# Performance work log

Measured on AMD Instinct MI355X. Metric: run time of the kernel, lower is better.

Reference implementation:

```python
import jax, jax.numpy as jnp
import numpy as np
from jax import lax

BETA = 0.9
THRESHOLD = 1.0
SLOPE = 25.0
TIME_STEPS = 50


@jax.custom_vjp
def spike(u):
    # Heaviside forward; fast_sigmoid surrogate backward
    return (u > 0).astype(u.dtype)

def _spike_fwd(u):
    return spike(u), u

def _spike_bwd(u, g):
    return (g / (SLOPE * jnp.abs(u) + 1.0) ** 2,)

spike.defvjp(_spike_fwd, _spike_bwd)


def setup_inputs() -> dict:
    key = jax.random.key(0)
    k = jax.random.split(key, 5)
    B, D_IN, D_H, D_OUT = 1024, 1024, 2048, 256
    return {
        "x": jax.random.normal(k[0], (B, D_IN), jnp.float32),
        "W1": jax.random.normal(k[1], (D_H, D_IN), jnp.float32) / np.sqrt(D_IN),
        "b1": jax.random.normal(k[2], (D_H,), jnp.float32) * 0.01,
        "W2": jax.random.normal(k[3], (D_OUT, D_H), jnp.float32) / np.sqrt(D_H),
        "b2": jax.random.normal(k[4], (D_OUT,), jnp.float32) * 0.01,
    }


def reference(x, W1, b1, W2, b2):
    # fc1(x) is constant across time steps (static input) -> hoist out of scan
    cur1 = x @ W1.T + b1  # [B, H]
    B = x.shape[0]
    H, O = W1.shape[0], W2.shape[0]
    dt = x.dtype

    def step(carry, _):
        mem1, mem2, h_sum, out_sum = carry
        # snntorch Leaky, subtract reset: reset based on PREVIOUS mem, detached
        reset1 = lax.stop_gradient((mem1 > THRESHOLD).astype(dt))
        mem1 = BETA * mem1 + cur1 - reset1 * THRESHOLD
        spk1 = spike(mem1 - THRESHOLD)
        cur2 = spk1 @ W2.T + b2  # [B, O]
        reset2 = lax.stop_gradient((mem2 > THRESHOLD).astype(dt))
        mem2 = BETA * mem2 + cur2 - reset2 * THRESHOLD
        spk2 = spike(mem2 - THRESHOLD)
        return (mem1, mem2, h_sum + spk1, out_sum + spk2), None

    init = (jnp.zeros((B, H), dt), jnp.zeros((B, O), dt),
            jnp.zeros((B, H), dt), jnp.zeros((B, O), dt))
    (mem1, mem2, h_sum, out_sum), _ = lax.scan(step, init, None, length=TIME_STEPS)
    return (h_sum, out_sum)
```

## Files before the change

kernel.cpp:

```cpp
#include <hip/hip_runtime.h>
#include <stdint.h>


#define BATCH 1024
#define DIN   1024
#define DH    2048
#define DOUT  256
#define TSTEPS 50
#define QS    131072.0f
#define QINVS 7.62939453125e-6f

typedef __bf16 bf16x8 __attribute__((ext_vector_type(8)));
typedef float  f32x4  __attribute__((ext_vector_type(4)));
typedef int    i32x4  __attribute__((ext_vector_type(4)));
typedef int    i32x16 __attribute__((ext_vector_type(16)));

__device__ __forceinline__ void gl2lds16(const void* g, void* l) {
  __builtin_amdgcn_global_load_lds(
      (const __attribute__((address_space(1))) uint32_t*)(uintptr_t)g,
      (__attribute__((address_space(3))) uint32_t*)(uint32_t)(uintptr_t)l,
      16, 0, 0);
}

__device__ __forceinline__ uint16_t f32_bf16_rne(float f) {
  uint32_t u = __float_as_uint(f);
  uint32_t r = u + 0x7FFFu + ((u >> 16) & 1u);
  return (uint16_t)(r >> 16);
}

__global__ void prep_kernel(const float* __restrict__ x, const float* __restrict__ W1,
                            const float* __restrict__ W2,
                            uint16_t* __restrict__ PXh, uint16_t* __restrict__ PXl,
                            uint16_t* __restrict__ PWh, uint16_t* __restrict__ PWl,
                            int8_t* __restrict__ PB) {
  int bid = blockIdx.x;
  if (bid < 1536) {
    const float* src;
    uint16_t *dh, *dl;
    int m, ko; size_t M;
    if (bid < 512) {
      int t = bid * 256 + threadIdx.x;
      m = t >> 7; ko = t & 127; M = 1024;
      src = x + (size_t)m * DIN + ko * 8;
      dh = PXh; dl = PXl;
    } else {
      int t = (bid - 512) * 256 + threadIdx.x;
      m = t >> 7; ko = t & 127; M = 2048;
      src = W1 + (size_t)m * DIN + ko * 8;
      dh = PWh; dl = PWl;
    }
    float4 a = *(const float4*)(src);
    float4 b = *(const float4*)(src + 4);
    float v[8] = {a.x, a.y, a.z, a.w, b.x, b.y, b.z, b.w};
    uint16_t h[8], l[8];
#pragma unroll
    for (int j = 0; j < 8; ++j) {
      h[j] = f32_bf16_rne(v[j]);
      l[j] = f32_bf16_rne(v[j] - __uint_as_float((uint32_t)h[j] << 16));
    }
    size_t o = ((size_t)ko * M + m) * 8;
    *(uint4*)(dh + o) = make_uint4(h[0] | (h[1] << 16), h[2] | (h[3] << 16),
                                   h[4] | (h[5] << 16), h[6] | (h[7] << 16));
    *(uint4*)(dl + o) = make_uint4(l[0] | (l[1] << 16), l[2] | (l[3] << 16),
                                   l[4] | (l[5] << 16), l[6] | (l[7] << 16));
  } else {
    int t = (bid - 1536) * 256 + threadIdx.x;
    int k0 = (t & 127) * 16;
    int n = t >> 7;
    uint32_t hw[4], lw[4];
#pragma unroll
    for (int g = 0; g < 4; ++g) {
      float4 v = *(const float4*)(W2 + (size_t)n * DH + k0 + g * 4);
      float vv[4] = {v.x, v.y, v.z, v.w};
      uint32_t hb = 0, lb = 0;
#pragma unroll
      for (int j = 0; j < 4; ++j) {
        int q = (int)rintf(vv[j] * QS);
        int h = (q + 128) >> 8;
        int l = q - (h << 8);
        hb |= ((uint32_t)(uint8_t)(int8_t)h) << (8 * j);
        lb |= ((uint32_t)(uint8_t)(int8_t)l) << (8 * j);
      }
      hw[g] = hb; lw[g] = lb;
    }
    int kc = k0 >> 5, kh = (k0 >> 4) & 1, nb = n >> 5;
    int lane = (n & 31) + 32 * kh;
    size_t off = (((size_t)(kc * 8 + nb) * 2 + 0) * 64 + lane) * 16;
    *(uint4*)(PB + off)        = make_uint4(hw[0], hw[1], hw[2], hw[3]);
    *(uint4*)(PB + off + 1024) = make_uint4(lw[0], lw[1], lw[2], lw[3]);
  }
}

__global__ __launch_bounds__(256, 4) void gemm1_kernel(
    const uint16_t* __restrict__ PXh, const uint16_t* __restrict__ PXl,
    const uint16_t* __restrict__ PWh, const uint16_t* __restrict__ PWl,
    const float* __restrict__ bias, float* __restrict__ C) {
  const int K = DIN, N = DH;
  __shared__ uint16_t sAh[2048], sAl[2048], sBh[2048], sBl[2048];
  int tid = threadIdx.x;
  int lane = tid & 63, wave = tid >> 6;
  int wm = (wave >> 1) * 32, wn = (wave & 1) * 32;
  int m0 = blockIdx.x * 64, n0 = blockIdx.y * 64;
  int rf = lane & 15;
  int ko = lane >> 4;

  f32x4 acc[2][2] = {};

  int sko = tid >> 6, srow = tid & 63;

  for (int k0 = 0; k0 < K; k0 += 32) {
    size_t oa = ((size_t)((k0 >> 3) + sko) * 1024 + m0 + srow) * 8;
    size_t ob = ((size_t)((k0 >> 3) + sko) * 2048 + n0 + srow) * 8;
    gl2lds16(PXh + oa, &sAh[tid * 8]);
    gl2lds16(PXl + oa, &sAl[tid * 8]);
    gl2lds16(PWh + ob, &sBh[tid * 8]);
    gl2lds16(PWl + ob, &sBl[tid * 8]);
    __syncthreads();

    bf16x8 ah[2], al[2], bh[2], bl[2];
#pragma unroll
    for (int i = 0; i < 2; ++i) {
      int ra = (ko * 64 + wm + i * 16 + rf) * 8;
      ah[i] = *(const bf16x8*)&sAh[ra];
      al[i] = *(const bf16x8*)&sAl[ra];
      int rb = (ko * 64 + wn + i * 16 + rf) * 8;
      bh[i] = *(const bf16x8*)&sBh[rb];
      bl[i] = *(const bf16x8*)&sBl[rb];
    }
#pragma unroll
    for (int i = 0; i < 2; ++i)
#pragma unroll
      for (int j = 0; j < 2; ++j) {
        acc[i][j] = __builtin_amdgcn_mfma_f32_16x16x32_bf16(ah[i], bh[j], acc[i][j], 0, 0, 0);
        acc[i][j] = __builtin_amdgcn_mfma_f32_16x16x32_bf16(ah[i], bl[j], acc[i][j], 0, 0, 0);
        acc[i][j] = __builtin_amdgcn_mfma_f32_16x16x32_bf16(al[i], bh[j], acc[i][j], 0, 0, 0);
      }
    __syncthreads();
  }

  int cq = (lane >> 4) * 4;
#pragma unroll
  for (int j = 0; j < 2; ++j) {
    int col = n0 + wn + j * 16 + rf;
    float bv = bias[col];
#pragma unroll
    for (int i = 0; i < 2; ++i) {
      size_t row = m0 + wm + i * 16 + cq;
      float* cp = C + row * N + col;
#pragma unroll
      for (int r = 0; r < 4; ++r) cp[(size_t)r * N] = acc[i][j][r] + bv;
    }
  }
}

__global__ __launch_bounds__(512, 2) void gemm2_kernel(
    const int8_t* __restrict__ PA, const int8_t* __restrict__ PB,
    const float* __restrict__ bias, float* __restrict__ C, int RB) {
  int tid = threadIdx.x;
  int lane = tid & 63, wave = tid >> 6;
  int wmh = wave >> 2;
  int wnq = wave & 3;
  int bx = blockIdx.x;
  int mb0 = bx * 4 + wmh * 2;

  const int8_t* pa = PA + ((size_t)mb0 * 64 + lane) * 16;
  const int8_t* pb = PB + ((size_t)wnq * 4 * 64 + lane) * 16;
  size_t strideA = (size_t)RB * 1024;

  i32x16 acch[2][2] = {};
  i32x16 accl[2][2] = {};

  i32x4 ab[4][2], bb[4][4];
#pragma unroll
  for (int u = 0; u < 4; ++u) {
    ab[u][0] = *(const i32x4*)(pa);
    ab[u][1] = *(const i32x4*)(pa + 1024);
    bb[u][0] = *(const i32x4*)(pb);
    bb[u][1] = *(const i32x4*)(pb + 1024);
    bb[u][2] = *(const i32x4*)(pb + 2048);
    bb[u][3] = *(const i32x4*)(pb + 3072);
    pa += strideA; pb += 16384;
  }
  __builtin_amdgcn_sched_barrier(0);

  for (int kc0 = 0; kc0 < 64; kc0 += 4) {
#pragma unroll
    for (int u = 0; u < 4; ++u) {
      acch[0][0] = __builtin_amdgcn_mfma_i32_32x32x32_i8(ab[u][0], bb[u][0], acch[0][0], 0, 0, 0);
      accl[0][0] = __builtin_amdgcn_mfma_i32_32x32x32_i8(ab[u][0], bb[u][1], accl[0][0], 0, 0, 0);
      acch[0][1] = __builtin_amdgcn_mfma_i32_32x32x32_i8(ab[u][0], bb[u][2], acch[0][1], 0, 0, 0);
      accl[0][1] = __builtin_amdgcn_mfma_i32_32x32x32_i8(ab[u][0], bb[u][3], accl[0][1], 0, 0, 0);
      acch[1][0] = __builtin_amdgcn_mfma_i32_32x32x32_i8(ab[u][1], bb[u][0], acch[1][0], 0, 0, 0);
      accl[1][0] = __builtin_amdgcn_mfma_i32_32x32x32_i8(ab[u][1], bb[u][1], accl[1][0], 0, 0, 0);
      acch[1][1] = __builtin_amdgcn_mfma_i32_32x32x32_i8(ab[u][1], bb[u][2], acch[1][1], 0, 0, 0);
      accl[1][1] = __builtin_amdgcn_mfma_i32_32x32x32_i8(ab[u][1], bb[u][3], accl[1][1], 0, 0, 0);
      __builtin_amdgcn_sched_barrier(0);
      ab[u][0] = *(const i32x4*)(pa);
      ab[u][1] = *(const i32x4*)(pa + 1024);
      bb[u][0] = *(const i32x4*)(pb);
      bb[u][1] = *(const i32x4*)(pb + 1024);
      bb[u][2] = *(const i32x4*)(pb + 2048);
      bb[u][3] = *(const i32x4*)(pb + 3072);
      pa += strideA; pb += 16384;
      __builtin_amdgcn_sched_barrier(0);
    }
  }

  int rm = lane & 31, half = lane >> 5;
#pragma unroll
  for (int mi = 0; mi < 2; ++mi)
#pragma unroll
    for (int ni = 0; ni < 2; ++ni) {
      int col = wnq * 64 + ni * 32 + rm;
      float bv = bias[col];
#pragma unroll
      for (int r = 0; r < 16; ++r) {
        int row = bx * 128 + wmh * 64 + mi * 32 + (r & 3) + 8 * (r >> 2) + 4 * half;
        int q = acch[mi][ni][r] * 256 + accl[mi][ni][r];
        C[(size_t)row * DOUT + col] = (float)q * QINVS + bv;
      }
    }
}

__global__ void lif1_kernel(const float* __restrict__ cur1, float* __restrict__ mem1,
                            int8_t* __restrict__ PA, float* __restrict__ hsum,
                            int tc, int init, int save_mem, int RB) {
#pragma clang fp contract(off)
  int idx = blockIdx.x * 256 + threadIdx.x;
  int b = idx & 1023;
  int h0 = (idx >> 10) * 16;
  size_t e0 = (size_t)b * DH + h0;

  float m[16], c[16], hs[16];
#pragma unroll
  for (int g = 0; g < 4; ++g) {
    float4 v = *(const float4*)(cur1 + e0 + g * 4);
    c[g * 4] = v.x; c[g * 4 + 1] = v.y; c[g * 4 + 2] = v.z; c[g * 4 + 3] = v.w;
  }
#pragma unroll
  for (int v = 0; v < 16; ++v) { m[v] = 0.0f; hs[v] = 0.0f; }
  if (!init) {
#pragma unroll
    for (int g = 0; g < 4; ++g) {
      float4 v = *(const float4*)(mem1 + e0 + g * 4);
      m[g * 4] = v.x; m[g * 4 + 1] = v.y; m[g * 4 + 2] = v.z; m[g * 4 + 3] = v.w;
    }
  }

  int kc = h0 >> 5, kh = (h0 >> 4) & 1;
  int lane = (b & 31) + 32 * kh;
  int8_t* pa = PA + (((size_t)kc * RB + (b >> 5)) * 64 + lane) * 16;

  for (int t = 0; t < tc; ++t) {
    uint32_t w[4] = {0, 0, 0, 0};
#pragma unroll
    for (int v = 0; v < 16; ++v) {
      float r = (m[v] > 1.0f) ? 1.0f : 0.0f;
      m[v] = 0.9f * m[v] + c[v] - r;
      bool s = (m[v] - 1.0f) > 0.0f;
      hs[v] += s ? 1.0f : 0.0f;
      w[v >> 2] |= (s ? 1u : 0u) << (8 * (v & 3));
    }
    *(uint4*)(pa + (size_t)t * 32768) = make_uint4(w[0], w[1], w[2], w[3]);
  }

  if (save_mem) {
#pragma unroll
    for (int g = 0; g < 4; ++g)
      *(float4*)(mem1 + e0 + g * 4) = make_float4(m[g * 4], m[g * 4 + 1], m[g * 4 + 2], m[g * 4 + 3]);
  }
  if (init) {
#pragma unroll
    for (int g = 0; g < 4; ++g)
      *(float4*)(hsum + e0 + g * 4) = make_float4(hs[g * 4], hs[g * 4 + 1], hs[g * 4 + 2], hs[g * 4 + 3]);
  } else {
#pragma unroll
    for (int g = 0; g < 4; ++g) {
      float4 v = *(float4*)(hsum + e0 + g * 4);
      v.x += hs[g * 4]; v.y += hs[g * 4 + 1]; v.z += hs[g * 4 + 2]; v.w += hs[g * 4 + 3];
      *(float4*)(hsum + e0 + g * 4) = v;
    }
  }
}

__global__ void lif2_kernel(const float* __restrict__ cur2, float* __restrict__ mem2,
                            float* __restrict__ osum, int tc, int init, int save_mem) {
#pragma clang fp contract(off)
  int idx = blockIdx.x * 256 + threadIdx.x;
  int e = idx * 4;
  float m[4], os[4];
  if (init) { m[0] = m[1] = m[2] = m[3] = 0.0f; }
  else { float4 v = *(const float4*)(mem2 + e); m[0] = v.x; m[1] = v.y; m[2] = v.z; m[3] = v.w; }
  os[0] = os[1] = os[2] = os[3] = 0.0f;
  for (int t = 0; t < tc; ++t) {
    float4 cv = *(const float4*)(cur2 + (size_t)t * (BATCH * DOUT) + e);
    float c[4] = {cv.x, cv.y, cv.z, cv.w};
#pragma unroll
    for (int v = 0; v < 4; ++v) {
      float r = (m[v] > 1.0f) ? 1.0f : 0.0f;
      m[v] = 0.9f * m[v] + c[v] - r;
      os[v] += ((m[v] - 1.0f) > 0.0f) ? 1.0f : 0.0f;
    }
  }
  if (save_mem) *(float4*)(mem2 + e) = make_float4(m[0], m[1], m[2], m[3]);
  if (init) {
    *(float4*)(osum + e) = make_float4(os[0], os[1], os[2], os[3]);
  } else {
    float4 v = *(float4*)(osum + e);
    v.x += os[0]; v.y += os[1]; v.z += os[2]; v.w += os[3];
    *(float4*)(osum + e) = v;
  }
}

extern "C" void kernel_launch(void* const* d_in, const int* in_sizes, int n_in,
                              void* d_out, int out_size, void* d_ws, size_t ws_size,
                              hipStream_t stream) {
  const float* x  = (const float*)d_in[0];
  const float* W1 = (const float*)d_in[1];
  const float* b1 = (const float*)d_in[2];
  const float* W2 = (const float*)d_in[3];
  const float* b2 = (const float*)d_in[4];
  float* out = (float*)d_out;
  char* ws = (char*)d_ws;

  const size_t fixed = 40 * 1024 * 1024;
  int tc = 10;
  if (ws_size >= fixed + 50ull * (2097152 + 1048576)) tc = 50;
  else if (ws_size >= fixed + 25ull * (2097152 + 1048576)) tc = 25;
  int nchunk = TSTEPS / tc;
  int RB = tc * 32;

  size_t off = 0;
  auto alloc = [&](size_t b) { size_t p = off; off = (off + b + 255) & ~(size_t)255; return p; };
  uint16_t* PXh  = (uint16_t*)(ws + alloc(2097152));
  uint16_t* PXl  = (uint16_t*)(ws + alloc(2097152));
  uint16_t* PWh  = (uint16_t*)(ws + alloc(4194304));
  uint16_t* PWl  = (uint16_t*)(ws + alloc(4194304));
  int8_t*   PB   = (int8_t*)(ws + alloc(1048576 + 65536));
  float*    cur1 = (float*)(ws + alloc(8388608));
  float*    mem1 = (float*)(ws + alloc(8388608));
  float*    mem2 = (float*)(ws + alloc(1048576));
  int8_t*   PA   = (int8_t*)(ws + alloc((size_t)tc * BATCH * DH + 4ull * RB * 1024));
  float*    cur2c = (float*)(ws + alloc((size_t)tc * BATCH * DOUT * 4));

  if (nchunk > 1) {
    hipMemsetAsync(mem1, 0, 8388608, stream);
    hipMemsetAsync(mem2, 0, 1048576, stream);
  }

  prep_kernel<<<1664, 256, 0, stream>>>(x, W1, W2, PXh, PXl, PWh, PWl, PB);

  gemm1_kernel<<<dim3(BATCH / 64, DH / 64), 256, 0, stream>>>(PXh, PXl, PWh, PWl, b1, cur1);

  int save = (nchunk > 1) ? 1 : 0;
  for (int c = 0; c < nchunk; ++c) {
    int init = (c == 0) ? 1 : 0;
    lif1_kernel<<<(BATCH * DH) / (256 * 16), 256, 0, stream>>>(
        cur1, mem1, PA, out, tc, init, save, RB);
    gemm2_kernel<<<(tc * BATCH) / 128, 512, 0, stream>>>(
        PA, PB, b2, cur2c, RB);
    lif2_kernel<<<(BATCH * DOUT) / (256 * 4), 256, 0, stream>>>(
        cur2c, mem2, out + BATCH * DH, tc, init, save);
  }
}
```

Before: 202.7 us.

## Bit-pack spike matrix and drop LDS staging in first GEMM

The spike activations passed from the LIF1 stage to the second GEMM are now stored as 16-bit bitmasks instead of one byte per spike. The GEMM expands them back into int8 MFMA operands in registers with a multiply-and-mask trick. This cuts the spike buffer traffic by a factor of eight in exchange for some extra ALU work per MFMA. Separately, gemm1 now loads its operands straight from global memory into registers with a two-stage software prefetch, with no LDS staging and no block barriers, and its launch bounds change. The workspace sizing is adjusted to match.

```diff
diff --git a/kernel.cpp b/kernel.cpp
--- a/kernel.cpp
+++ b/kernel.cpp
@@ -15,17 +15,19 @@
 typedef int    i32x4  __attribute__((ext_vector_type(4)));
 typedef int    i32x16 __attribute__((ext_vector_type(16)));
 
-__device__ __forceinline__ void gl2lds16(const void* g, void* l) {
-  __builtin_amdgcn_global_load_lds(
-      (const __attribute__((address_space(1))) uint32_t*)(uintptr_t)g,
-      (__attribute__((address_space(3))) uint32_t*)(uint32_t)(uintptr_t)l,
-      16, 0, 0);
-}
-
 __device__ __forceinline__ uint16_t f32_bf16_rne(float f) {
   uint32_t u = __float_as_uint(f);
   uint32_t r = u + 0x7FFFu + ((u >> 16) & 1u);
   return (uint16_t)(r >> 16);
+}
+
+__device__ __forceinline__ i32x4 expand16(uint32_t s) {
+  i32x4 r;
+  r[0] = (int)((( s        & 0xFu) * 0x00204081u) & 0x01010101u);
+  r[1] = (int)((((s >>  4) & 0xFu) * 0x00204081u) & 0x01010101u);
+  r[2] = (int)((((s >>  8) & 0xFu) * 0x00204081u) & 0x01010101u);
+  r[3] = (int)((((s >> 12) & 0xFu) * 0x00204081u) & 0x01010101u);
+  return r;
 }
 
 __global__ void prep_kernel(const float* __restrict__ x, const float* __restrict__ W1,
@@ -91,61 +93,73 @@
   }
 }
 
-__global__ __launch_bounds__(256, 4) void gemm1_kernel(
+__global__ __launch_bounds__(256, 2) void gemm1_kernel(
     const uint16_t* __restrict__ PXh, const uint16_t* __restrict__ PXl,
     const uint16_t* __restrict__ PWh, const uint16_t* __restrict__ PWl,
     const float* __restrict__ bias, float* __restrict__ C) {
-  const int K = DIN, N = DH;
-  __shared__ uint16_t sAh[2048], sAl[2048], sBh[2048], sBl[2048];
+  const int N = DH;
   int tid = threadIdx.x;
   int lane = tid & 63, wave = tid >> 6;
   int wm = (wave >> 1) * 32, wn = (wave & 1) * 32;
-  int m0 = blockIdx.x * 64, n0 = blockIdx.y * 64;
+  int m0 = blockIdx.x * 64 + wm;
+  int n0 = blockIdx.y * 64 + wn;
   int rf = lane & 15;
   int ko = lane >> 4;
+  const int AK = 4 * 1024 * 8;
+  const int BK = 4 * 2048 * 8;
+
+  const uint16_t* axh = PXh + ((size_t)ko * 1024 + m0 + rf) * 8;
+  const uint16_t* axl = PXl + ((size_t)ko * 1024 + m0 + rf) * 8;
+  const uint16_t* bwh = PWh + ((size_t)ko * 2048 + n0 + rf) * 8;
+  const uint16_t* bwl = PWl + ((size_t)ko * 2048 + n0 + rf) * 8;
 
   f32x4 acc[2][2] = {};
-
-  int sko = tid >> 6, srow = tid & 63;
-
-  for (int k0 = 0; k0 < K; k0 += 32) {
-    size_t oa = ((size_t)((k0 >> 3) + sko) * 1024 + m0 + srow) * 8;
-    size_t ob = ((size_t)((k0 >> 3) + sko) * 2048 + n0 + srow) * 8;
-    gl2lds16(PXh + oa, &sAh[tid * 8]);
-    gl2lds16(PXl + oa, &sAl[tid * 8]);
-    gl2lds16(PWh + ob, &sBh[tid * 8]);
-    gl2lds16(PWl + ob, &sBl[tid * 8]);
-    __syncthreads();
-
-    bf16x8 ah[2], al[2], bh[2], bl[2];
+  bf16x8 ah[2][2], al[2][2], bh[2][2], bl[2][2];
+#pragma unroll
+  for (int s = 0; s < 2; ++s) {
 #pragma unroll
     for (int i = 0; i < 2; ++i) {
-      int ra = (ko * 64 + wm + i * 16 + rf) * 8;
-      ah[i] = *(const bf16x8*)&sAh[ra];
-      al[i] = *(const bf16x8*)&sAl[ra];
-      int rb = (ko * 64 + wn + i * 16 + rf) * 8;
-      bh[i] = *(const bf16x8*)&sBh[rb];
-      bl[i] = *(const bf16x8*)&sBl[rb];
-    }
-#pragma unroll
-    for (int i = 0; i < 2; ++i)
-#pragma unroll
-      for (int j = 0; j < 2; ++j) {
-        acc[i][j] = __builtin_amdgcn_mfma_f32_16x16x32_bf16(ah[i], bh[j], acc[i][j], 0, 0, 0);
-        acc[i][j] = __builtin_amdgcn_mfma_f32_16x16x32_bf16(ah[i], bl[j], acc[i][j], 0, 0, 0);
-        acc[i][j] = __builtin_amdgcn_mfma_f32_16x16x32_bf16(al[i], bh[j], acc[i][j], 0, 0, 0);
+      ah[s][i] = *(const bf16x8*)(axh + i * 128);
+      al[s][i] = *(const bf16x8*)(axl + i * 128);
+      bh[s][i] = *(const bf16x8*)(bwh + i * 128);
+      bl[s][i] = *(const bf16x8*)(bwl + i * 128);
+    }
+    axh += AK; axl += AK; bwh += BK; bwl += BK;
+  }
+  __builtin_amdgcn_sched_barrier(0);
+
+  for (int kc0 = 0; kc0 < 32; kc0 += 2) {
+#pragma unroll
+    for (int u = 0; u < 2; ++u) {
+#pragma unroll
+      for (int i = 0; i < 2; ++i)
+#pragma unroll
+        for (int j = 0; j < 2; ++j) {
+          acc[i][j] = __builtin_amdgcn_mfma_f32_16x16x32_bf16(ah[u][i], bh[u][j], acc[i][j], 0, 0, 0);
+          acc[i][j] = __builtin_amdgcn_mfma_f32_16x16x32_bf16(ah[u][i], bl[u][j], acc[i][j], 0, 0, 0);
+          acc[i][j] = __builtin_amdgcn_mfma_f32_16x16x32_bf16(al[u][i], bh[u][j], acc[i][j], 0, 0, 0);
+        }
+      __builtin_amdgcn_sched_barrier(0);
+#pragma unroll
+      for (int i = 0; i < 2; ++i) {
+        ah[u][i] = *(const bf16x8*)(axh + i * 128);
+        al[u][i] = *(const bf16x8*)(axl + i * 128);
+        bh[u][i] = *(const bf16x8*)(bwh + i * 128);
+        bl[u][i] = *(const bf16x8*)(bwl + i * 128);
       }
-    __syncthreads();
+      axh += AK; axl += AK; bwh += BK; bwl += BK;
+      __builtin_amdgcn_sched_barrier(0);
+    }
   }
 
   int cq = (lane >> 4) * 4;
 #pragma unroll
   for (int j = 0; j < 2; ++j) {
-    int col = n0 + wn + j * 16 + rf;
+    int col = n0 + j * 16 + rf;
     float bv = bias[col];
 #pragma unroll
     for (int i = 0; i < 2; ++i) {
-      size_t row = m0 + wm + i * 16 + cq;
+      size_t row = m0 + i * 16 + cq;
       float* cp = C + row * N + col;
 #pragma unroll
       for (int r = 0; r < 4; ++r) cp[(size_t)r * N] = acc[i][j][r] + bv;
@@ -154,7 +168,7 @@
 }
 
 __global__ __launch_bounds__(512, 2) void gemm2_kernel(
-    const int8_t* __restrict__ PA, const int8_t* __restrict__ PB,
+    const uint16_t* __restrict__ PAb, const int8_t* __restrict__ PB,
     const float* __restrict__ bias, float* __restrict__ C, int RB) {
   int tid = threadIdx.x;
   int lane = tid & 63, wave = tid >> 6;
@@ -163,18 +177,19 @@
   int bx = blockIdx.x;
   int mb0 = bx * 4 + wmh * 2;
 
-  const int8_t* pa = PA + ((size_t)mb0 * 64 + lane) * 16;
-  const int8_t* pb = PB + ((size_t)wnq * 4 * 64 + lane) * 16;
-  size_t strideA = (size_t)RB * 1024;
+  const uint16_t* pa = PAb + (size_t)mb0 * 64 + lane;
+  const int8_t*   pb = PB + ((size_t)wnq * 4 * 64 + lane) * 16;
+  size_t strideA = (size_t)RB * 64;
 
   i32x16 acch[2][2] = {};
   i32x16 accl[2][2] = {};
 
-  i32x4 ab[4][2], bb[4][4];
+  uint32_t abit[4][2];
+  i32x4 bb[4][4];
 #pragma unroll
   for (int u = 0; u < 4; ++u) {
-    ab[u][0] = *(const i32x4*)(pa);
-    ab[u][1] = *(const i32x4*)(pa + 1024);
+    abit[u][0] = pa[0];
+    abit[u][1] = pa[64];
     bb[u][0] = *(const i32x4*)(pb);
     bb[u][1] = *(const i32x4*)(pb + 1024);
     bb[u][2] = *(const i32x4*)(pb + 2048);
@@ -186,17 +201,19 @@
   for (int kc0 = 0; kc0 < 64; kc0 += 4) {
 #pragma unroll
     for (int u = 0; u < 4; ++u) {
-      acch[0][0] = __builtin_amdgcn_mfma_i32_32x32x32_i8(ab[u][0], bb[u][0], acch[0][0], 0, 0, 0);
-      accl[0][0] = __builtin_amdgcn_mfma_i32_32x32x32_i8(ab[u][0], bb[u][1], accl[0][0], 0, 0, 0);
-      acch[0][1] = __builtin_amdgcn_mfma_i32_32x32x32_i8(ab[u][0], bb[u][2], acch[0][1], 0, 0, 0);
-      accl[0][1] = __builtin_amdgcn_mfma_i32_32x32x32_i8(ab[u][0], bb[u][3], accl[0][1], 0, 0, 0);
-      acch[1][0] = __builtin_amdgcn_mfma_i32_32x32x32_i8(ab[u][1], bb[u][0], acch[1][0], 0, 0, 0);
-      accl[1][0] = __builtin_amdgcn_mfma_i32_32x32x32_i8(ab[u][1], bb[u][1], accl[1][0], 0, 0, 0);
-      acch[1][1] = __builtin_amdgcn_mfma_i32_32x32x32_i8(ab[u][1], bb[u][2], acch[1][1], 0, 0, 0);
-      accl[1][1] = __builtin_amdgcn_mfma_i32_32x32x32_i8(ab[u][1], bb[u][3], accl[1][1], 0, 0, 0);
+      i32x4 a0 = expand16(abit[u][0]);
+      i32x4 a1 = expand16(abit[u][1]);
+      acch[0][0] = __builtin_amdgcn_mfma_i32_32x32x32_i8(a0, bb[u][0], acch[0][0], 0, 0, 0);
+      accl[0][0] = __builtin_amdgcn_mfma_i32_32x32x32_i8(a0, bb[u][1], accl[0][0], 0, 0, 0);
+      acch[0][1] = __builtin_amdgcn_mfma_i32_32x32x32_i8(a0, bb[u][2], acch[0][1], 0, 0, 0);
+      accl[0][1] = __builtin_amdgcn_mfma_i32_32x32x32_i8(a0, bb[u][3], accl[0][1], 0, 0, 0);
+      acch[1][0] = __builtin_amdgcn_mfma_i32_32x32x32_i8(a1, bb[u][0], acch[1][0], 0, 0, 0);
+      accl[1][0] = __builtin_amdgcn_mfma_i32_32x32x32_i8(a1, bb[u][1], accl[1][0], 0, 0, 0);
+      acch[1][1] = __builtin_amdgcn_mfma_i32_32x32x32_i8(a1, bb[u][2], acch[1][1], 0, 0, 0);
+      accl[1][1] = __builtin_amdgcn_mfma_i32_32x32x32_i8(a1, bb[u][3], accl[1][1], 0, 0, 0);
       __builtin_amdgcn_sched_barrier(0);
-      ab[u][0] = *(const i32x4*)(pa);
-      ab[u][1] = *(const i32x4*)(pa + 1024);
+      abit[u][0] = pa[0];
+      abit[u][1] = pa[64];
       bb[u][0] = *(const i32x4*)(pb);
       bb[u][1] = *(const i32x4*)(pb + 1024);
       bb[u][2] = *(const i32x4*)(pb + 2048);
@@ -223,7 +240,7 @@
 }
 
 __global__ void lif1_kernel(const float* __restrict__ cur1, float* __restrict__ mem1,
-                            int8_t* __restrict__ PA, float* __restrict__ hsum,
+                            uint16_t* __restrict__ PAb, float* __restrict__ hsum,
                             int tc, int init, int save_mem, int RB) {
 #pragma clang fp contract(off)
   int idx = blockIdx.x * 256 + threadIdx.x;
@@ -249,19 +266,20 @@
 
   int kc = h0 >> 5, kh = (h0 >> 4) & 1;
   int lane = (b & 31) + 32 * kh;
-  int8_t* pa = PA + (((size_t)kc * RB + (b >> 5)) * 64 + lane) * 16;
+  uint16_t* pab = PAb + ((size_t)kc * RB + (b >> 5)) * 64 + lane;
 
   for (int t = 0; t < tc; ++t) {
-    uint32_t w[4] = {0, 0, 0, 0};
+    uint32_t w = 0;
 #pragma unroll
     for (int v = 0; v < 16; ++v) {
       float r = (m[v] > 1.0f) ? 1.0f : 0.0f;
       m[v] = 0.9f * m[v] + c[v] - r;
       bool s = (m[v] - 1.0f) > 0.0f;
       hs[v] += s ? 1.0f : 0.0f;
-      w[v >> 2] |= (s ? 1u : 0u) << (8 * (v & 3));
-    }
-    *(uint4*)(pa + (size_t)t * 32768) = make_uint4(w[0], w[1], w[2], w[3]);
+      w |= (s ? 1u : 0u) << v;
+    }
+    *pab = (uint16_t)w;
+    pab += 32 * 64;
   }
 
   if (save_mem) {
@@ -323,10 +341,11 @@
   float* out = (float*)d_out;
   char* ws = (char*)d_ws;
 
-  const size_t fixed = 40 * 1024 * 1024;
+  const size_t fixed = 36 * 1024 * 1024;
+  const size_t perT  = 262144 + 1048576;
   int tc = 10;
-  if (ws_size >= fixed + 50ull * (2097152 + 1048576)) tc = 50;
-  else if (ws_size >= fixed + 25ull * (2097152 + 1048576)) tc = 25;
+  if (ws_size >= fixed + 50ull * perT) tc = 50;
+  else if (ws_size >= fixed + 25ull * perT) tc = 25;
   int nchunk = TSTEPS / tc;
   int RB = tc * 32;
 
@@ -336,11 +355,11 @@
   uint16_t* PXl  = (uint16_t*)(ws + alloc(2097152));
   uint16_t* PWh  = (uint16_t*)(ws + alloc(4194304));
   uint16_t* PWl  = (uint16_t*)(ws + alloc(4194304));
-  int8_t*   PB   = (int8_t*)(ws + alloc(1048576 + 65536));
+  int8_t*   PB   = (int8_t*)(ws + alloc(1048576 + 262144));
   float*    cur1 = (float*)(ws + alloc(8388608));
   float*    mem1 = (float*)(ws + alloc(8388608));
   float*    mem2 = (float*)(ws + alloc(1048576));
-  int8_t*   PA   = (int8_t*)(ws + alloc((size_t)tc * BATCH * DH + 4ull * RB * 1024));
+  uint16_t* PAb  = (uint16_t*)(ws + alloc((size_t)tc * 262144 + 4ull * RB * 128));
   float*    cur2c = (float*)(ws + alloc((size_t)tc * BATCH * DOUT * 4));
 
   if (nchunk > 1) {
@@ -350,15 +369,15 @@
 
   prep_kernel<<<1664, 256, 0, stream>>>(x, W1, W2, PXh, PXl, PWh, PWl, PB);
 
-  gemm1_kernel<<<dim3(BATCH / 64, DH / 64), 256, 0, stream>>>(PXh, PXl, PWh, PWl, b1, cur1);
+  gemm1_kernel<<<dim3(16, 32), 256, 0, stream>>>(PXh, PXl, PWh, PWl, b1, cur1);
 
   int save = (nchunk > 1) ? 1 : 0;
   for (int c = 0; c < nchunk; ++c) {
     int init = (c == 0) ? 1 : 0;
     lif1_kernel<<<(BATCH * DH) / (256 * 16), 256, 0, stream>>>(
-        cur1, mem1, PA, out, tc, init, save, RB);
+        cur1, mem1, PAb, out, tc, init, save, RB);
     gemm2_kernel<<<(tc * BATCH) / 128, 512, 0, stream>>>(
-        PA, PB, b2, cur2c, RB);
+        PAb, PB, b2, cur2c, RB);
     lif2_kernel<<<(BATCH * DOUT) / (256 * 4), 256, 0, stream>>>(
         cur2c, mem2, out + BATCH * DH, tc, init, save);
   }
```

Result: no change. 206.2 us (+1.7%).
